# Optimization experiments

Measured on AMD Instinct MI355X. Metric: run time of the kernel, lower is better.

The kernel has to match this reference:

```python
import jax, jax.numpy as jnp
import numpy as np
from jax.scipy.special import gammaln

L, R, W0, W1, B = 100, 3, 5, 20, 50


def mish(x):
    return x * jnp.tanh(jax.nn.softplus(x))


def conv1d(x, w, b):
    y = jax.lax.conv_general_dilated(x, w, (1,), 'VALID', dimension_numbers=('NCH', 'OIH', 'NCH'))
    return y + b[None, :, None]


def maxpool2(x):
    n = (x.shape[-1] // 2) * 2
    return x[..., :n].reshape(x.shape[0], x.shape[1], -1, 2).max(-1)


def dir_lp(x, alpha):
    # Dirichlet(alpha) log-prob over last dim, capped at 3.0 as in pwm_pr_lp/gamma_pr_lp
    K = x.shape[-1]
    lp = ((alpha - 1.0) * jnp.log(x)).sum(-1) + gammaln(K * alpha) - K * gammaln(alpha)
    return jnp.minimum(3.0, lp)


def binom_lp(n, k):
    # Binomial(n, 0.5) log pmf
    return gammaln(n + 1.0) - gammaln(k + 1.0) - gammaln(n - k + 1.0) + n * jnp.log(0.5)


def dlog_lp(a, b, mean, s, x):
    # DiscreteLogistic on [a,b]; log_prob evaluated at shifted value x (true value v = x + a)
    v = x + a
    up = jnp.where(v >= b, 1.0, jax.nn.sigmoid((v + 0.5 - mean) / s))
    lo = jnp.where(v <= a, 0.0, jax.nn.sigmoid((v - 0.5 - mean) / s))
    return jnp.log(up - lo + 1e-12)


def elbo(pwm_logits, wn_W1, wn_b1, wn_W2, wn_b2, wn_W3, wn_b3,
         gn_c1W, gn_c1b, gn_c2W, gn_c2b, gn_l1W, gn_l1b, gn_l2W, gn_l2b,
         zn_c1W, zn_c1b, zn_c2W, zn_c2b, zn_clsW, zn_clsb, zn_delW, zn_delb, X):
    pwm = jax.nn.softmax(pwm_logits, -1)              # [R,W1,4] PWM probabilities
    pwm_log = jnp.log(pwm)
    log_prior = dir_lp(pwm, 0.2).sum()
    # w guide net (Dropout inactive at eval)
    h = mish(wn_W1[0] + wn_b1)
    h = mish(h @ wn_W2 + wn_b2)
    ww = jax.nn.sigmoid(h @ wn_W3 + wn_b3)            # [R]
    mean = ww * (W1 - W0) + W0
    # cartesian product of floor/ceil per motif (torch.cartesian_prod: first var slowest)
    bits = (jnp.arange(8)[:, None] >> jnp.arange(2, -1, -1)[None, :]) & 1
    w2f = jnp.where(bits == 1, jnp.ceil(mean)[None, :], jnp.floor(mean)[None, :])  # [8,R]
    w_lp = dlog_lp(float(W0), float(W1), mean[None, :], 0.05, w2f - W0)            # [8,R]
    w_prob = jnp.exp(w_lp).T                                                        # [R,8]
    log_prior = log_prior + jnp.dot(w_prob.prod(0), binom_lp(float(W1 - W0), w2f).sum(1))
    log_guide = jnp.dot(w_prob.prod(0), w_lp.sum(1))
    # S[b,j,p,k] = log pwm[j,k,X[b,p+k]] -- replaces diag_embed + conv1d + log
    pidx = jnp.clip(jnp.arange(L)[:, None] + jnp.arange(W1)[None, :], 0, L - 1)
    Xoh = jax.nn.one_hot(X[:, pidx], 4, dtype=pwm.dtype)                            # [B,L,W1,4]
    S = jnp.einsum('bpkc,jkc->bjpk', Xoh, pwm_log)                                  # [B,R,L,W1]
    q = jnp.arange(L)
    kk = jnp.arange(W1)
    log_X = jnp.float32(0.0)
    for i_w in range(2 ** R):
        w = w2f[i_w].astype(jnp.int32)                                              # [R]
        kmask = (kk[None, :] < w[:, None]).astype(S.dtype)                          # [R,W1]
        ymid = (S * kmask[None, :, None, :]).sum(-1) / w.astype(S.dtype)[None, :, None]
        left = (w - 1) // 2
        valid = (q[None, :] >= left[:, None]) & (q[None, :] <= left[:, None] + (L - w)[:, None])
        src = jnp.clip(q[None, :] - left[:, None], 0, L - 1)
        ysh = jnp.take_along_axis(ymid, jnp.broadcast_to(src[None], ymid.shape), axis=2)
        y = jnp.where(valid[None], ysh, 0.0)                                        # [B,R,L]
        # gamma_net
        g = maxpool2(mish(conv1d(y, gn_c1W, gn_c1b)))
        g = maxpool2(mish(conv1d(g, gn_c2W, gn_c2b))).reshape(B, -1)                # [B,22]
        g = mish(g @ gn_l1W + gn_l1b)
        gamma = jax.nn.softmax(g @ gn_l2W + gn_l2b, -1)                             # [B,R]
        log_prior = log_prior + w_prob[:, i_w].prod() * dir_lp(gamma, 0.2).sum()
        for I in range(R):
            wI = w[I]
            I_pr = gamma[:, I]
            # z_net
            z = maxpool2(mish(conv1d(y[:, I:I + 1, :], zn_c1W, zn_c1b)))
            z = maxpool2(mish(conv1d(z, zn_c2W, zn_c2b))).reshape(B, -1)            # [B,176]
            Z_cls = z @ zn_clsW + zn_clsb                                           # [B,9]
            Z_del = jax.nn.sigmoid(z @ zn_delW + zn_delb)                           # [B,10]
            ind = jnp.argmax(Z_cls, 1) + 1
            gap = (99 - W1) / 10.0
            Z_m = (ind.astype(S.dtype) + Z_del[jnp.arange(B), ind]) * gap
            Z2 = jnp.stack([jnp.floor(Z_m), jnp.ceil(Z_m)], 0).astype(jnp.int32)    # [2,B]
            Z2f = Z2.astype(S.dtype)
            Z_lp = dlog_lp(0.0, 99.0, Z_m[None], 0.05, Z2f)
            Z_prob = jnp.exp(Z_lp)
            log_prior = log_prior + (w_prob[I, i_w] * Z_prob * I_pr[None] * binom_lp(float(L - W1 - 1), Z2f)).sum()
            log_guide = log_guide + (w_prob[I, i_w] * Z_prob * I_pr[None] * Z_lp).sum()
            # log_X: vectorized per-sample gather of pwm[I, k, X[i, Z+k]] for k < wI
            pos = jnp.clip(Z2[:, :, None] + kk[None, None, :], 0, L - 1)            # [2,B,W1]
            Xs = X[jnp.arange(B)[None, :, None], pos]                               # [2,B,W1]
            val = pwm_log[I][kk[None, None, :], Xs]                                 # [2,B,W1]
            lpv = (val * (kk[None, None, :] < wI)).sum(-1)                          # [2,B]
            log_X = log_X + w_prob[I, i_w] * (Z_prob * I_pr[None] * lpv).sum()
    return -log_X - log_prior + log_guide


def setup_inputs() -> dict:
    key = jax.random.key(0)
    ks = jax.random.split(key, 32)
    def n(i, shape, s=0.1):
        return (jax.random.normal(ks[i], shape) * s).astype(jnp.float32)
    return {
        'pwm_logits': n(0, (R, W1, 4), 0.5),
        'wn_W1': n(1, (1, 16)), 'wn_b1': n(2, (16,)),
        'wn_W2': n(3, (16, 16)), 'wn_b2': n(4, (16,)),
        'wn_W3': n(5, (16, 3), 0.01), 'wn_b3': n(6, (3,), 0.01),
        'gn_c1W': n(7, (16, 3, 5)), 'gn_c1b': n(8, (16,)),
        'gn_c2W': n(9, (1, 16, 5)), 'gn_c2b': n(10, (1,)),
        'gn_l1W': n(11, (22, 16)), 'gn_l1b': n(12, (16,)),
        'gn_l2W': n(13, (16, 3)), 'gn_l2b': n(14, (3,)),
        'zn_c1W': n(15, (16, 1, 5)), 'zn_c1b': n(16, (16,)),
        'zn_c2W': n(17, (8, 16, 5)), 'zn_c2b': n(18, (8,)),
        'zn_clsW': n(19, (176, 9)), 'zn_clsb': n(20, (9,)),
        'zn_delW': n(21, (176, 10)), 'zn_delb': n(22, (10,)),
        'X': jax.random.randint(ks[23], (B, L), 0, 4, dtype=jnp.int32),
    }


def reference(pwm_logits, wn_W1, wn_b1, wn_W2, wn_b2, wn_W3, wn_b3,
              gn_c1W, gn_c1b, gn_c2W, gn_c2b, gn_l1W, gn_l1b, gn_l2W, gn_l2b,
              zn_c1W, zn_c1b, zn_c2W, zn_c2b, zn_clsW, zn_clsb, zn_delW, zn_delb, X):
    return elbo(pwm_logits, wn_W1, wn_b1, wn_W2, wn_b2, wn_W3, wn_b3,
                gn_c1W, gn_c1b, gn_c2W, gn_c2b, gn_l1W, gn_l1b, gn_l2W, gn_l2b,
                zn_c1W, zn_c1b, zn_c2W, zn_c2b, zn_clsW, zn_clsb, zn_delW, zn_delb, X)
```

## Files before the change

### kernel.cpp

```cpp
#include <hip/hip_runtime.h>
#include <math.h>

#define LN2F 0.69314718055994530942f

#define WS_GAMMA 0
#define WS_ZT    1200

__device__ __forceinline__ float sigm(float x){ return 1.0f/(1.0f+expf(-x)); }
__device__ __forceinline__ float mishf(float x){
    if (x >= 30.0f) return x;
    float w = expf(x);
    float u = 1.0f + w; u *= u;
    return x * (u - 1.0f) / (u + 1.0f);
}

__global__ __launch_bounds__(256) void kMain(
    const float* __restrict__ pwm_logits,
    const float* __restrict__ wn_W1, const float* __restrict__ wn_b1,
    const float* __restrict__ wn_W2, const float* __restrict__ wn_b2,
    const float* __restrict__ wn_W3, const float* __restrict__ wn_b3,
    const float* __restrict__ gc1W, const float* __restrict__ gc1b,
    const float* __restrict__ gc2W, const float* __restrict__ gc2b,
    const float* __restrict__ gl1W, const float* __restrict__ gl1b,
    const float* __restrict__ gl2W, const float* __restrict__ gl2b,
    const float* __restrict__ zc1W, const float* __restrict__ zc1b,
    const float* __restrict__ zc2W, const float* __restrict__ zc2b,
    const float* __restrict__ zclsW, const float* __restrict__ zclsb,
    const float* __restrict__ zdelW, const float* __restrict__ zdelb,
    const int* __restrict__ X, float* __restrict__ ws)
{
    int tid=threadIdx.x, bid=blockIdx.x;
    bool isC = bid < 400;
    int iw=0, b, It=0, I=0;
    if(isC){ iw=bid%8; b=bid/8; }
    else   { int idx=bid-400; It=idx%6; b=idx/6; I=It>>1; }

    __shared__ float pl[240];
    __shared__ int   xs[100];
    __shared__ float h1[16], h2[16], wv6[6];
    __shared__ float ybuf[3][100];
    __shared__ float w1buf[240];
    __shared__ float zw2[640];
    __shared__ float hp[16][48];
    __shared__ float c2o[8][44];
    __shared__ float zz[176];
    __shared__ float cls[9], del[10];
    __shared__ float g22[22], h16[16];

    if(tid<60){
        const float* l=pwm_logits+tid*4;
        float m=fmaxf(fmaxf(l[0],l[1]),fmaxf(l[2],l[3]));
        float se=expf(l[0]-m)+expf(l[1]-m)+expf(l[2]-m)+expf(l[3]-m);
        float ls=logf(se);
        for(int c=0;c<4;c++) pl[tid*4+c]=l[c]-m-ls;
    }
    if(tid>=64 && tid<164) xs[tid-64]=X[b*100+tid-64];
    if(tid>=192 && tid<208) h1[tid-192]=mishf(wn_W1[tid-192]+wn_b1[tid-192]);
    __syncthreads();
    if(tid<16){
        float a=wn_b2[tid];
        for(int i=0;i<16;i++) a+=h1[i]*wn_W2[i*16+tid];
        h2[tid]=mishf(a);
    }
    __syncthreads();
    if(tid<6){
        int j=tid>>1;
        float a=wn_b3[j];
        for(int i=0;i<16;i++) a+=h2[i]*wn_W3[i*3+j];
        float mean=sigm(a)*15.0f+5.0f;
        wv6[tid]=(tid&1)?ceilf(mean):floorf(mean);
    }
    if(isC){ for(int i=tid;i<240;i+=256) w1buf[i]=gc1W[i]; }
    else{
        for(int i=tid;i<80;i+=256)  w1buf[i]=zc1W[i];
        for(int i=tid;i<640;i+=256) zw2[i]=zc2W[i];
    }
    __syncthreads();

    int np = isC ? 3 : 1;
    for(int idx=tid; idx<np*100; idx+=256){
        int jj=idx/100, q=idx%100;
        int j = isC ? jj : I;
        int t = isC ? ((iw>>(2-jj))&1) : (It&1);
        int w=(int)wv6[j*2+t];
        int left=(w-1)>>1;
        float yv=0.0f;
        if(q>=left && q<=left+100-w){
            int src=q-left;
            float s=0.0f;
            const float* pj=&pl[j*80];
            for(int k=0;k<w;k++) s+=pj[k*4+xs[src+k]];
            yv=s/(float)w;
        }
        ybuf[jj][q]=yv;
    }
    __syncthreads();

    if(isC){
        for(int idx=tid; idx<768; idx+=256){
            int o=idx/48, p2=idx%48;
            const float* wr=&w1buf[o*15];
            float bo=gc1b[o], m=-1e30f;
            for(int d=0;d<2;d++){
                int p=2*p2+d;
                float acc=bo;
                for(int i=0;i<3;i++)
                    for(int k=0;k<5;k++) acc+=ybuf[i][p+k]*wr[i*5+k];
                m=fmaxf(m,mishf(acc));
            }
            hp[o][p2]=m;
        }
        __syncthreads();
        if(tid<44){
            float acc=gc2b[0];
            for(int i=0;i<16;i++)
                for(int k=0;k<5;k++) acc+=hp[i][tid+k]*gc2W[i*5+k];
            c2o[0][tid]=mishf(acc);
        }
        __syncthreads();
        if(tid<22) g22[tid]=fmaxf(c2o[0][2*tid],c2o[0][2*tid+1]);
        __syncthreads();
        if(tid<16){
            float acc=gl1b[tid];
            for(int i=0;i<22;i++) acc+=g22[i]*gl1W[i*16+tid];
            h16[tid]=mishf(acc);
        }
        __syncthreads();
        if(tid==0){
            float o3[3], m=-1e30f;
            for(int o=0;o<3;o++){
                float acc=gl2b[o];
                for(int i=0;i<16;i++) acc+=h16[i]*gl2W[i*3+o];
                o3[o]=acc; m=fmaxf(m,acc);
            }
            float se=0.0f;
            for(int o=0;o<3;o++){ o3[o]=expf(o3[o]-m); se+=o3[o]; }
            float inv=1.0f/se;
            for(int o=0;o<3;o++) ws[WS_GAMMA+(iw*50+b)*3+o]=o3[o]*inv;
        }
    } else {
        for(int idx=tid; idx<768; idx+=256){
            int o=idx/48, p2=idx%48;
            const float* wr=&w1buf[o*5];
            float bo=zc1b[o], m=-1e30f;
            for(int d=0;d<2;d++){
                int p=2*p2+d;
                float acc=bo;
                for(int k=0;k<5;k++) acc+=ybuf[0][p+k]*wr[k];
                m=fmaxf(m,mishf(acc));
            }
            hp[o][p2]=m;
        }
        __syncthreads();
        for(int idx=tid; idx<352; idx+=256){
            int o=idx/44, p=idx%44;
            float acc=zc2b[o];
            for(int i=0;i<16;i++)
                for(int k=0;k<5;k++) acc+=hp[i][p+k]*zw2[(o*16+i)*5+k];
            c2o[o][p]=mishf(acc);
        }
        __syncthreads();
        if(tid<176){
            int o=tid/22, q=tid%22;
            zz[tid]=fmaxf(c2o[o][2*q],c2o[o][2*q+1]);
        }
        __syncthreads();
        if(tid<9){
            float acc=zclsb[tid];
            for(int m2=0;m2<176;m2++) acc+=zz[m2]*zclsW[m2*9+tid];
            cls[tid]=acc;
        }
        if(tid>=64 && tid<74){
            int n=tid-64;
            float acc=zdelb[n];
            for(int m2=0;m2<176;m2++) acc+=zz[m2]*zdelW[m2*10+n];
            del[n]=sigm(acc);
        }
        __syncthreads();
        if(tid==0){
            int ind=0; float best=cls[0];
            for(int n=1;n<9;n++) if(cls[n]>best){best=cls[n];ind=n;}
            ind+=1;
            float Zm=((float)ind+del[ind])*7.9f;
            int wI=(int)wv6[It];
            float r0=0,r1=0,r2=0;
            const float* pI=&pl[I*80];
            for(int s=0;s<2;s++){
                float zf=s?ceilf(Zm):floorf(Zm);
                float up=(zf>=99.0f)?1.0f:sigm((zf+0.5f-Zm)*20.0f);
                float lo=(zf<=0.0f)?0.0f:sigm((zf-0.5f-Zm)*20.0f);
                float zlp=logf(up-lo+1e-12f);
                float zp=expf(zlp);
                float bin=lgammaf(80.0f)-lgammaf(zf+1.0f)-lgammaf(80.0f-zf)-79.0f*LN2F;
                int zi=(int)zf;
                float lpv=0.0f;
                for(int k=0;k<wI;k++){
                    int p=zi+k; if(p>99)p=99;
                    lpv+=pI[k*4+xs[p]];
                }
                r0+=zp*bin; r1+=zp*zlp; r2+=zp*lpv;
            }
            ws[WS_ZT+    It*50+b]=r0;
            ws[WS_ZT+300+It*50+b]=r1;
            ws[WS_ZT+600+It*50+b]=r2;
        }
    }
}

__global__ __launch_bounds__(256) void kFin(
    const float* __restrict__ pwm_logits,
    const float* __restrict__ wn_W1, const float* __restrict__ wn_b1,
    const float* __restrict__ wn_W2, const float* __restrict__ wn_b2,
    const float* __restrict__ wn_W3, const float* __restrict__ wn_b3,
    const float* __restrict__ ws, float* __restrict__ out)
{
    __shared__ float sa[256], sb[256], sc[256];
    __shared__ float h1[16], h2[16];
    __shared__ float pjt[6], wlp6[6], bin6[6];
    __shared__ float wprod[8];
    __shared__ float bp_s, bg_s;
    int tid=threadIdx.x;
    float C4=lgammaf(0.8f)-4.0f*lgammaf(0.2f);
    float C3=lgammaf(0.6f)-3.0f*lgammaf(0.2f);

    float part=0.0f;
    if(tid<60){
        const float* l=pwm_logits+tid*4;
        float m=fmaxf(fmaxf(l[0],l[1]),fmaxf(l[2],l[3]));
        float se=expf(l[0]-m)+expf(l[1]-m)+expf(l[2]-m)+expf(l[3]-m);
        float ls=logf(se);
        float dsum=0.0f;
        for(int c=0;c<4;c++) dsum+=l[c]-m-ls;
        part=fminf(3.0f, -0.8f*dsum+C4);
    }
    sa[tid]=part;
    if(tid<16) h1[tid]=mishf(wn_W1[tid]+wn_b1[tid]);
    __syncthreads();
    for(int s=128;s>0;s>>=1){ if(tid<s) sa[tid]+=sa[tid+s]; __syncthreads(); }
    float dirsum = sa[0];
    if(tid<16){
        float a=wn_b2[tid];
        for(int i=0;i<16;i++) a+=h1[i]*wn_W2[i*16+tid];
        h2[tid]=mishf(a);
    }
    __syncthreads();
    if(tid<6){
        int j=tid>>1;
        float a=wn_b3[j];
        for(int i=0;i<16;i++) a+=h2[i]*wn_W3[i*3+j];
        float mean=sigm(a)*15.0f+5.0f;
        float wv=(tid&1)?ceilf(mean):floorf(mean);
        float up=(wv>=20.0f)?1.0f:sigm((wv+0.5f-mean)*20.0f);
        float lo=(wv<=5.0f)?0.0f:sigm((wv-0.5f-mean)*20.0f);
        wlp6[tid]=logf(up-lo+1e-12f);
        pjt[tid]=expf(wlp6[tid]);
        bin6[tid]=lgammaf(16.0f)-lgammaf(wv+1.0f)-lgammaf(16.0f-wv)-15.0f*LN2F;
    }
    __syncthreads();
    if(tid==0){
        float bp=dirsum, bg=0.0f;
        for(int i=0;i<8;i++){
            int b0=(i>>2)&1, b1=(i>>1)&1, b2=i&1;
            float wp=pjt[b0]*pjt[2+b1]*pjt[4+b2];
            wprod[i]=wp;
            bp+=wp*(bin6[b0]+bin6[2+b1]+bin6[4+b2]);
            bg+=wp*(wlp6[b0]+wlp6[2+b1]+wlp6[4+b2]);
        }
        bp_s=bp; bg_s=bg;
    }
    __syncthreads();

    float pp=0.0f, pg=0.0f, px=0.0f;
    for(int idx=tid; idx<400; idx+=256){
        int iw=idx/50, b=idx%50;
        const float* g=&ws[WS_GAMMA+(iw*50+b)*3];
        float lp=-0.8f*(logf(g[0])+logf(g[1])+logf(g[2]))+C3;
        pp += wprod[iw]*fminf(3.0f,lp);
    }
    for(int idx=tid; idx<300; idx+=256){
        int It=idx/50, b=idx%50;
        int I=It>>1, t=It&1;
        float gs=0.0f;
        for(int iw=0;iw<8;iw++)
            if(((iw>>(2-I))&1)==t) gs+=ws[WS_GAMMA+(iw*50+b)*3+I];
        float G=pjt[It]*gs;
        pp += G*ws[WS_ZT+idx];
        pg += G*ws[WS_ZT+300+idx];
        px += G*ws[WS_ZT+600+idx];
    }
    sa[tid]=pp; sb[tid]=pg; sc[tid]=px;
    __syncthreads();
    for(int s=128;s>0;s>>=1){
        if(tid<s){ sa[tid]+=sa[tid+s]; sb[tid]+=sb[tid+s]; sc[tid]+=sc[tid+s]; }
        __syncthreads();
    }
    if(tid==0){
        float log_prior=bp_s+sa[0];
        float log_guide=bg_s+sb[0];
        out[0] = -sc[0] - log_prior + log_guide;
    }
}

extern "C" void kernel_launch(void* const* d_in, const int* in_sizes, int n_in,
                              void* d_out, int out_size, void* d_ws, size_t ws_size,
                              hipStream_t stream)
{
    const float* pwm_logits=(const float*)d_in[0];
    const float* wn_W1 =(const float*)d_in[1];
    const float* wn_b1 =(const float*)d_in[2];
    const float* wn_W2 =(const float*)d_in[3];
    const float* wn_b2 =(const float*)d_in[4];
    const float* wn_W3 =(const float*)d_in[5];
    const float* wn_b3 =(const float*)d_in[6];
    const float* gn_c1W=(const float*)d_in[7];
    const float* gn_c1b=(const float*)d_in[8];
    const float* gn_c2W=(const float*)d_in[9];
    const float* gn_c2b=(const float*)d_in[10];
    const float* gn_l1W=(const float*)d_in[11];
    const float* gn_l1b=(const float*)d_in[12];
    const float* gn_l2W=(const float*)d_in[13];
    const float* gn_l2b=(const float*)d_in[14];
    const float* zn_c1W=(const float*)d_in[15];
    const float* zn_c1b=(const float*)d_in[16];
    const float* zn_c2W=(const float*)d_in[17];
    const float* zn_c2b=(const float*)d_in[18];
    const float* zn_clsW=(const float*)d_in[19];
    const float* zn_clsb=(const float*)d_in[20];
    const float* zn_delW=(const float*)d_in[21];
    const float* zn_delb=(const float*)d_in[22];
    const int*   X     =(const int*)d_in[23];
    float* ws =(float*)d_ws;
    float* out=(float*)d_out;

    hipLaunchKernelGGL(kMain, dim3(700), dim3(256), 0, stream,
                       pwm_logits, wn_W1, wn_b1, wn_W2, wn_b2, wn_W3, wn_b3,
                       gn_c1W, gn_c1b, gn_c2W, gn_c2b, gn_l1W, gn_l1b, gn_l2W, gn_l2b,
                       zn_c1W, zn_c1b, zn_c2W, zn_c2b, zn_clsW, zn_clsb, zn_delW, zn_delb,
                       X, ws);
    hipLaunchKernelGGL(kFin, dim3(1),   dim3(256), 0, stream,
                       pwm_logits, wn_W1, wn_b1, wn_W2, wn_b2, wn_W3, wn_b3, ws, out);
}
```

Before: 124.3 us.

## Hoist shared prologue into pre-kernel, fuse final reduction via last-block atomic

```diff
diff --git a/kernel.cpp b/kernel.cpp
--- a/kernel.cpp
+++ b/kernel.cpp
@@ -3,8 +3,15 @@
 
 #define LN2F 0.69314718055994530942f
 
-#define WS_GAMMA 0
-#define WS_ZT    1200
+#define WS_PL    0
+#define WS_WV    240
+#define WS_PJT   246
+#define WS_WPROD 252
+#define WS_BASEP 260
+#define WS_BASEG 261
+#define WS_CNT   262
+#define WS_GAMMA 272
+#define WS_ZT    1472
 
 __device__ __forceinline__ float sigm(float x){ return 1.0f/(1.0f+expf(-x)); }
 __device__ __forceinline__ float mishf(float x){
@@ -14,11 +21,65 @@
     return x * (u - 1.0f) / (u + 1.0f);
 }
 
-__global__ __launch_bounds__(256) void kMain(
+__global__ __launch_bounds__(64) void kPre(
     const float* __restrict__ pwm_logits,
     const float* __restrict__ wn_W1, const float* __restrict__ wn_b1,
     const float* __restrict__ wn_W2, const float* __restrict__ wn_b2,
     const float* __restrict__ wn_W3, const float* __restrict__ wn_b3,
+    float* __restrict__ ws)
+{
+    __shared__ float h1[16], h2[16];
+    __shared__ float wlp6[6], pjt6[6], bin6[6];
+    int tid=threadIdx.x;
+    float C4=lgammaf(0.8f)-4.0f*lgammaf(0.2f);
+    float part=0.0f;
+    if(tid<60){
+        const float* l=pwm_logits+tid*4;
+        float m=fmaxf(fmaxf(l[0],l[1]),fmaxf(l[2],l[3]));
+        float se=expf(l[0]-m)+expf(l[1]-m)+expf(l[2]-m)+expf(l[3]-m);
+        float ls=logf(se);
+        float d=0.0f;
+        for(int c=0;c<4;c++){ float v=l[c]-m-ls; ws[WS_PL+tid*4+c]=v; d+=v; }
+        part=fminf(3.0f,-0.8f*d+C4);
+    }
+    for(int off=32;off>0;off>>=1) part += __shfl_down(part,off);
+    if(tid<16) h1[tid]=mishf(wn_W1[tid]+wn_b1[tid]);
+    __syncthreads();
+    if(tid<16){
+        float a=wn_b2[tid];
+        for(int i=0;i<16;i++) a+=h1[i]*wn_W2[i*16+tid];
+        h2[tid]=mishf(a);
+    }
+    __syncthreads();
+    if(tid<6){
+        int j=tid>>1;
+        float a=wn_b3[j];
+        for(int i=0;i<16;i++) a+=h2[i]*wn_W3[i*3+j];
+        float mean=sigm(a)*15.0f+5.0f;
+        float wv=(tid&1)?ceilf(mean):floorf(mean);
+        float up=(wv>=20.0f)?1.0f:sigm((wv+0.5f-mean)*20.0f);
+        float lo=(wv<=5.0f)?0.0f:sigm((wv-0.5f-mean)*20.0f);
+        float wl=logf(up-lo+1e-12f);
+        wlp6[tid]=wl; pjt6[tid]=expf(wl);
+        bin6[tid]=lgammaf(16.0f)-lgammaf(wv+1.0f)-lgammaf(16.0f-wv)-15.0f*LN2F;
+        ws[WS_WV+tid]=wv; ws[WS_PJT+tid]=pjt6[tid];
+    }
+    __syncthreads();
+    if(tid==0){
+        float bp=part, bg=0.0f;
+        for(int i=0;i<8;i++){
+            int b0=(i>>2)&1,b1=(i>>1)&1,b2=i&1;
+            float wp=pjt6[b0]*pjt6[2+b1]*pjt6[4+b2];
+            ws[WS_WPROD+i]=wp;
+            bp+=wp*(bin6[b0]+bin6[2+b1]+bin6[4+b2]);
+            bg+=wp*(wlp6[b0]+wlp6[2+b1]+wlp6[4+b2]);
+        }
+        ws[WS_BASEP]=bp; ws[WS_BASEG]=bg;
+        ((unsigned int*)ws)[WS_CNT]=0u;
+    }
+}
+
+__global__ __launch_bounds__(256) void kAll(
     const float* __restrict__ gc1W, const float* __restrict__ gc1b,
     const float* __restrict__ gc2W, const float* __restrict__ gc2b,
     const float* __restrict__ gl1W, const float* __restrict__ gl1b,
@@ -27,49 +88,35 @@
     const float* __restrict__ zc2W, const float* __restrict__ zc2b,
     const float* __restrict__ zclsW, const float* __restrict__ zclsb,
     const float* __restrict__ zdelW, const float* __restrict__ zdelb,
-    const int* __restrict__ X, float* __restrict__ ws)
+    const int* __restrict__ X, float* __restrict__ ws, float* __restrict__ out)
 {
     int tid=threadIdx.x, bid=blockIdx.x;
-    bool isC = bid < 400;
+    bool isC = bid<400;
     int iw=0, b, It=0, I=0;
-    if(isC){ iw=bid%8; b=bid/8; }
+    if(isC){ iw=bid&7; b=bid>>3; }
     else   { int idx=bid-400; It=idx%6; b=idx/6; I=It>>1; }
 
     __shared__ float pl[240];
     __shared__ int   xs[100];
-    __shared__ float h1[16], h2[16], wv6[6];
+    __shared__ float wv6s[6], pjt6s[6], wpr8s[8], base2s[2];
     __shared__ float ybuf[3][100];
     __shared__ float w1buf[240];
     __shared__ float zw2[640];
     __shared__ float hp[16][48];
     __shared__ float c2o[8][44];
     __shared__ float zz[176];
+    __shared__ float pcl[72], pdl[80];
     __shared__ float cls[9], del[10];
     __shared__ float g22[22], h16[16];
-
-    if(tid<60){
-        const float* l=pwm_logits+tid*4;
-        float m=fmaxf(fmaxf(l[0],l[1]),fmaxf(l[2],l[3]));
-        float se=expf(l[0]-m)+expf(l[1]-m)+expf(l[2]-m)+expf(l[3]-m);
-        float ls=logf(se);
-        for(int c=0;c<4;c++) pl[tid*4+c]=l[c]-m-ls;
-    }
-    if(tid>=64 && tid<164) xs[tid-64]=X[b*100+tid-64];
-    if(tid>=192 && tid<208) h1[tid-192]=mishf(wn_W1[tid-192]+wn_b1[tid-192]);
-    __syncthreads();
-    if(tid<16){
-        float a=wn_b2[tid];
-        for(int i=0;i<16;i++) a+=h1[i]*wn_W2[i*16+tid];
-        h2[tid]=mishf(a);
-    }
-    __syncthreads();
-    if(tid<6){
-        int j=tid>>1;
-        float a=wn_b3[j];
-        for(int i=0;i<16;i++) a+=h2[i]*wn_W3[i*3+j];
-        float mean=sigm(a)*15.0f+5.0f;
-        wv6[tid]=(tid&1)?ceilf(mean):floorf(mean);
-    }
+    __shared__ float zmS;
+    __shared__ int   lastFlag;
+
+    for(int i=tid;i<240;i+=256) pl[i]=ws[WS_PL+i];
+    if(tid<100) xs[tid]=X[b*100+tid];
+    if(tid>=240&&tid<246) wv6s[tid-240]=ws[WS_WV+tid-240];
+    if(tid>=246&&tid<252) pjt6s[tid-246]=ws[WS_PJT+tid-246];
+    if(tid>=224&&tid<232) wpr8s[tid-224]=ws[WS_WPROD+tid-224];
+    if(tid>=232&&tid<234) base2s[tid-232]=ws[WS_BASEP+tid-232];
     if(isC){ for(int i=tid;i<240;i+=256) w1buf[i]=gc1W[i]; }
     else{
         for(int i=tid;i<80;i+=256)  w1buf[i]=zc1W[i];
@@ -82,7 +129,7 @@
         int jj=idx/100, q=idx%100;
         int j = isC ? jj : I;
         int t = isC ? ((iw>>(2-jj))&1) : (It&1);
-        int w=(int)wv6[j*2+t];
+        int w=(int)wv6s[j*2+t];
         int left=(w-1)>>1;
         float yv=0.0f;
         if(q>=left && q<=left+100-w){
@@ -165,139 +212,95 @@
             zz[tid]=fmaxf(c2o[o][2*q],c2o[o][2*q+1]);
         }
         __syncthreads();
-        if(tid<9){
-            float acc=zclsb[tid];
-            for(int m2=0;m2<176;m2++) acc+=zz[m2]*zclsW[m2*9+tid];
-            cls[tid]=acc;
-        }
-        if(tid>=64 && tid<74){
-            int n=tid-64;
-            float acc=zdelb[n];
-            for(int m2=0;m2<176;m2++) acc+=zz[m2]*zdelW[m2*10+n];
-            del[n]=sigm(acc);
-        }
+        if(tid<72){
+            int o=tid>>3, p=tid&7; int m0=p*22;
+            float a=0.0f;
+            for(int i2=0;i2<22;i2++) a+=zz[m0+i2]*zclsW[(m0+i2)*9+o];
+            pcl[tid]=a;
+        } else if(tid<152){
+            int t2=tid-72; int n=t2>>3, p=t2&7; int m0=p*22;
+            float a=0.0f;
+            for(int i2=0;i2<22;i2++) a+=zz[m0+i2]*zdelW[(m0+i2)*10+n];
+            pdl[t2]=a;
+        }
+        __syncthreads();
+        if(tid<9){ float a=zclsb[tid]; for(int p=0;p<8;p++) a+=pcl[tid*8+p]; cls[tid]=a; }
+        if(tid>=32&&tid<42){ int n=tid-32; float a=zdelb[n]; for(int p=0;p<8;p++) a+=pdl[n*8+p]; del[n]=sigm(a); }
         __syncthreads();
         if(tid==0){
             int ind=0; float best=cls[0];
-            for(int n=1;n<9;n++) if(cls[n]>best){best=cls[n];ind=n;}
+            for(int n2=1;n2<9;n2++) if(cls[n2]>best){best=cls[n2];ind=n2;}
             ind+=1;
-            float Zm=((float)ind+del[ind])*7.9f;
-            int wI=(int)wv6[It];
-            float r0=0,r1=0,r2=0;
+            zmS=((float)ind+del[ind])*7.9f;
+        }
+        __syncthreads();
+        if(tid<64){
+            float Zm=zmS; int wI=(int)wv6s[It];
+            int s=tid>>5, k=tid&31;
+            float zf = s?ceilf(Zm):floorf(Zm);
+            float up=(zf>=99.0f)?1.0f:sigm((zf+0.5f-Zm)*20.0f);
+            float lo=(zf<=0.0f)?0.0f:sigm((zf-0.5f-Zm)*20.0f);
+            float zlp=logf(up-lo+1e-12f);
+            float zp=expf(zlp);
+            float bin=lgammaf(80.0f)-lgammaf(zf+1.0f)-lgammaf(80.0f-zf)-79.0f*LN2F;
+            int zi=(int)zf;
             const float* pI=&pl[I*80];
-            for(int s=0;s<2;s++){
-                float zf=s?ceilf(Zm):floorf(Zm);
-                float up=(zf>=99.0f)?1.0f:sigm((zf+0.5f-Zm)*20.0f);
-                float lo=(zf<=0.0f)?0.0f:sigm((zf-0.5f-Zm)*20.0f);
-                float zlp=logf(up-lo+1e-12f);
-                float zp=expf(zlp);
-                float bin=lgammaf(80.0f)-lgammaf(zf+1.0f)-lgammaf(80.0f-zf)-79.0f*LN2F;
-                int zi=(int)zf;
-                float lpv=0.0f;
-                for(int k=0;k<wI;k++){
-                    int p=zi+k; if(p>99)p=99;
-                    lpv+=pI[k*4+xs[p]];
-                }
-                r0+=zp*bin; r1+=zp*zlp; r2+=zp*lpv;
+            float lpv=0.0f;
+            if(k<wI){ int p=zi+k; if(p>99)p=99; lpv=pI[k*4+xs[p]]; }
+            for(int off=16;off>0;off>>=1) lpv += __shfl_down(lpv,off);
+            float zp1=__shfl(zp,32), zlp1=__shfl(zlp,32), bin1=__shfl(bin,32), lpv1=__shfl(lpv,32);
+            if(tid==0){
+                ws[WS_ZT+    It*50+b]=zp*bin +zp1*bin1;
+                ws[WS_ZT+300+It*50+b]=zp*zlp +zp1*zlp1;
+                ws[WS_ZT+600+It*50+b]=zp*lpv +zp1*lpv1;
             }
-            ws[WS_ZT+    It*50+b]=r0;
-            ws[WS_ZT+300+It*50+b]=r1;
-            ws[WS_ZT+600+It*50+b]=r2;
-        }
-    }
-}
-
-__global__ __launch_bounds__(256) void kFin(
-    const float* __restrict__ pwm_logits,
-    const float* __restrict__ wn_W1, const float* __restrict__ wn_b1,
-    const float* __restrict__ wn_W2, const float* __restrict__ wn_b2,
-    const float* __restrict__ wn_W3, const float* __restrict__ wn_b3,
-    const float* __restrict__ ws, float* __restrict__ out)
-{
-    __shared__ float sa[256], sb[256], sc[256];
-    __shared__ float h1[16], h2[16];
-    __shared__ float pjt[6], wlp6[6], bin6[6];
-    __shared__ float wprod[8];
-    __shared__ float bp_s, bg_s;
-    int tid=threadIdx.x;
-    float C4=lgammaf(0.8f)-4.0f*lgammaf(0.2f);
+        }
+    }
+
+    __syncthreads();
+    if(tid==0){
+        __threadfence();
+        unsigned int old=atomicAdd((unsigned int*)ws+WS_CNT,1u);
+        lastFlag=(old==699u)?1:0;
+    }
+    __syncthreads();
+    if(!lastFlag) return;
+    __threadfence();
+
+    float* red=&hp[0][0];
     float C3=lgammaf(0.6f)-3.0f*lgammaf(0.2f);
-
-    float part=0.0f;
-    if(tid<60){
-        const float* l=pwm_logits+tid*4;
-        float m=fmaxf(fmaxf(l[0],l[1]),fmaxf(l[2],l[3]));
-        float se=expf(l[0]-m)+expf(l[1]-m)+expf(l[2]-m)+expf(l[3]-m);
-        float ls=logf(se);
-        float dsum=0.0f;
-        for(int c=0;c<4;c++) dsum+=l[c]-m-ls;
-        part=fminf(3.0f, -0.8f*dsum+C4);
-    }
-    sa[tid]=part;
-    if(tid<16) h1[tid]=mishf(wn_W1[tid]+wn_b1[tid]);
-    __syncthreads();
-    for(int s=128;s>0;s>>=1){ if(tid<s) sa[tid]+=sa[tid+s]; __syncthreads(); }
-    float dirsum = sa[0];
-    if(tid<16){
-        float a=wn_b2[tid];
-        for(int i=0;i<16;i++) a+=h1[i]*wn_W2[i*16+tid];
-        h2[tid]=mishf(a);
-    }
-    __syncthreads();
-    if(tid<6){
-        int j=tid>>1;
-        float a=wn_b3[j];
-        for(int i=0;i<16;i++) a+=h2[i]*wn_W3[i*3+j];
-        float mean=sigm(a)*15.0f+5.0f;
-        float wv=(tid&1)?ceilf(mean):floorf(mean);
-        float up=(wv>=20.0f)?1.0f:sigm((wv+0.5f-mean)*20.0f);
-        float lo=(wv<=5.0f)?0.0f:sigm((wv-0.5f-mean)*20.0f);
-        wlp6[tid]=logf(up-lo+1e-12f);
-        pjt[tid]=expf(wlp6[tid]);
-        bin6[tid]=lgammaf(16.0f)-lgammaf(wv+1.0f)-lgammaf(16.0f-wv)-15.0f*LN2F;
-    }
-    __syncthreads();
-    if(tid==0){
-        float bp=dirsum, bg=0.0f;
-        for(int i=0;i<8;i++){
-            int b0=(i>>2)&1, b1=(i>>1)&1, b2=i&1;
-            float wp=pjt[b0]*pjt[2+b1]*pjt[4+b2];
-            wprod[i]=wp;
-            bp+=wp*(bin6[b0]+bin6[2+b1]+bin6[4+b2]);
-            bg+=wp*(wlp6[b0]+wlp6[2+b1]+wlp6[4+b2]);
-        }
-        bp_s=bp; bg_s=bg;
-    }
-    __syncthreads();
-
     float pp=0.0f, pg=0.0f, px=0.0f;
     for(int idx=tid; idx<400; idx+=256){
-        int iw=idx/50, b=idx%50;
-        const float* g=&ws[WS_GAMMA+(iw*50+b)*3];
+        int iw2=idx/50, b2=idx%50;
+        const float* g=&ws[WS_GAMMA+(iw2*50+b2)*3];
         float lp=-0.8f*(logf(g[0])+logf(g[1])+logf(g[2]))+C3;
-        pp += wprod[iw]*fminf(3.0f,lp);
+        pp+=wpr8s[iw2]*fminf(3.0f,lp);
     }
     for(int idx=tid; idx<300; idx+=256){
-        int It=idx/50, b=idx%50;
-        int I=It>>1, t=It&1;
+        int It2=idx/50, b2=idx%50;
+        int I2=It2>>1, t2=It2&1;
         float gs=0.0f;
-        for(int iw=0;iw<8;iw++)
-            if(((iw>>(2-I))&1)==t) gs+=ws[WS_GAMMA+(iw*50+b)*3+I];
-        float G=pjt[It]*gs;
-        pp += G*ws[WS_ZT+idx];
-        pg += G*ws[WS_ZT+300+idx];
-        px += G*ws[WS_ZT+600+idx];
-    }
-    sa[tid]=pp; sb[tid]=pg; sc[tid]=px;
-    __syncthreads();
-    for(int s=128;s>0;s>>=1){
-        if(tid<s){ sa[tid]+=sa[tid+s]; sb[tid]+=sb[tid+s]; sc[tid]+=sc[tid+s]; }
+        for(int iw2=0;iw2<8;iw2++)
+            if(((iw2>>(2-I2))&1)==t2) gs+=ws[WS_GAMMA+(iw2*50+b2)*3+I2];
+        float G=pjt6s[It2]*gs;
+        pp+=G*ws[WS_ZT+idx];
+        pg+=G*ws[WS_ZT+300+idx];
+        px+=G*ws[WS_ZT+600+idx];
+    }
+    red[tid]=pp; red[256+tid]=pg; red[512+tid]=px;
+    __syncthreads();
+    for(int s2=128;s2>0;s2>>=1){
+        if(tid<s2){
+            red[tid]+=red[tid+s2];
+            red[256+tid]+=red[256+tid+s2];
+            red[512+tid]+=red[512+tid+s2];
+        }
         __syncthreads();
     }
     if(tid==0){
-        float log_prior=bp_s+sa[0];
-        float log_guide=bg_s+sb[0];
-        out[0] = -sc[0] - log_prior + log_guide;
+        float log_prior=base2s[0]+red[0];
+        float log_guide=base2s[1]+red[256];
+        out[0] = -red[512] - log_prior + log_guide;
     }
 }
 
@@ -332,11 +335,10 @@
     float* ws =(float*)d_ws;
     float* out=(float*)d_out;
 
-    hipLaunchKernelGGL(kMain, dim3(700), dim3(256), 0, stream,
-                       pwm_logits, wn_W1, wn_b1, wn_W2, wn_b2, wn_W3, wn_b3,
+    hipLaunchKernelGGL(kPre, dim3(1),   dim3(64),  0, stream,
+                       pwm_logits, wn_W1, wn_b1, wn_W2, wn_b2, wn_W3, wn_b3, ws);
+    hipLaunchKernelGGL(kAll, dim3(700), dim3(256), 0, stream,
                        gn_c1W, gn_c1b, gn_c2W, gn_c2b, gn_l1W, gn_l1b, gn_l2W, gn_l2b,
                        zn_c1W, zn_c1b, zn_c2W, zn_c2b, zn_clsW, zn_clsb, zn_delW, zn_delb,
-                       X, ws);
-    hipLaunchKernelGGL(kFin, dim3(1),   dim3(256), 0, stream,
-                       pwm_logits, wn_W1, wn_b1, wn_W2, wn_b2, wn_W3, wn_b3, ws, out);
+                       X, ws, out);
 }
```

After: 127.5 us. 2.6% more time.
